# Kernel optimization log

Measured on AMD Instinct MI355X. Metric: run time of the kernel, lower is better.

Reference implementation:

```python
import jax, jax.numpy as jnp
import numpy as np

EPS = 1e-05
N_HEADS = 16
HEAD_DIM = 64

def rms_norm(x, w, eps=EPS):
    # RMSNorm over last dim, computed in float32 then cast back (matches torch source)
    xf = x.astype(jnp.float32)
    out = xf * jax.lax.rsqrt(jnp.mean(xf * xf, axis=-1, keepdims=True) + eps)
    return (out * w).astype(x.dtype)

def split_heads(x, heads):
    # Faithful to reshape_heads: (B,T,C) -> (B,T,C//heads,heads) -> (B,heads,T,C//heads)
    B, T, C = x.shape
    return x.reshape(B, T, C // heads, heads).transpose(0, 3, 1, 2)

def setup_inputs() -> dict:
    key = jax.random.key(0)
    ks = jax.random.split(key, 5)
    B, T, D = 2, 2048, 1024
    s = 0.02
    return {
        "x": jax.random.normal(ks[0], (B, T, D), dtype=jnp.float32),
        "wq": jax.random.normal(ks[1], (D, N_HEADS * HEAD_DIM), dtype=jnp.float32) * s,
        "wk": jax.random.normal(ks[2], (D, N_HEADS * HEAD_DIM), dtype=jnp.float32) * s,
        "wv": jax.random.normal(ks[3], (D, N_HEADS * HEAD_DIM), dtype=jnp.float32) * s,
        "wo": jax.random.normal(ks[4], (N_HEADS * HEAD_DIM, D), dtype=jnp.float32) * s,
        "q_norm_w": jnp.ones((HEAD_DIM,), dtype=jnp.float32),
        "k_norm_w": jnp.ones((HEAD_DIM,), dtype=jnp.float32),
    }

def reference(x, wq, wk, wv, wo, q_norm_w, k_norm_w):
    B, T, D = x.shape
    # QKV projections (no bias)
    q = split_heads(x @ wq, N_HEADS)   # [B,H,T,hd]
    k = split_heads(x @ wk, N_HEADS)
    v = split_heads(x @ wv, N_HEADS)
    # per-head qk RMSNorm
    q = rms_norm(q, q_norm_w)
    k = rms_norm(k, k_norm_w)
    # scaled dot-product attention
    scale = 1.0 / jnp.sqrt(jnp.array(HEAD_DIM, dtype=x.dtype))
    scores = jnp.einsum('bhqd,bhkd->bhqk', q, k) * scale  # [B,H,T,T]
    attn = jax.nn.softmax(scores, axis=-1)
    out = jnp.einsum('bhqk,bhkd->bhqd', attn, v)           # [B,H,T,hd]
    # rearrange 'b h n d -> b n (h d)'
    out = out.transpose(0, 2, 1, 3).reshape(B, T, N_HEADS * HEAD_DIM)
    return out @ wo
```

## Files before the change

### kernel.cpp

```cpp
#include <hip/hip_runtime.h>
#include <hip/hip_fp16.h>

typedef _Float16 f16;
typedef _Float16 f16x8 __attribute__((ext_vector_type(8)));
typedef _Float16 f16x4 __attribute__((ext_vector_type(4)));
typedef float    f32x4 __attribute__((ext_vector_type(4)));

#define DEV __device__ __forceinline__

static constexpr int Tn = 2048;
static constexpr int Dn = 1024;
static constexpr int Hn = 16;
static constexpr int HDn = 64;
static constexpr int Mn = 2 * Tn;
static constexpr int NQKV = 3 * Dn;

DEV void gld16(const void* g, void* l) {
  __builtin_amdgcn_global_load_lds((const __attribute__((address_space(1))) unsigned int*)g,
                                   (__attribute__((address_space(3))) unsigned int*)l, 16, 0, 0);
}

__global__ __launch_bounds__(256) void k_cast_x(const float* __restrict__ x, f16* __restrict__ xb) {
  int i = blockIdx.x * 256 + threadIdx.x;
  float4 v = ((const float4*)x)[i];
  f16x4 o; o.x = (f16)v.x; o.y = (f16)v.y; o.z = (f16)v.z; o.w = (f16)v.w;
  ((f16x4*)xb)[i] = o;
}

__global__ __launch_bounds__(256) void k_wtrans(const float* __restrict__ wq, const float* __restrict__ wk,
                                                const float* __restrict__ wv, const float* __restrict__ wo,
                                                f16* __restrict__ wcat_t, f16* __restrict__ wot) {
  __shared__ float tile[64][65];
  const float* srcs[4] = {wq, wk, wv, wo};
  const float* w = srcs[blockIdx.z];
  f16* dst = (blockIdx.z == 3) ? wot : wcat_t + (size_t)blockIdx.z * Dn * Dn;
  int k0 = blockIdx.x * 64, n0 = blockIdx.y * 64;
#pragma unroll
  for (int p = 0; p < 16; ++p) {
    int flat = threadIdx.x + p * 256;
    int kl = flat >> 6, nl = flat & 63;
    tile[kl][nl] = w[(size_t)(k0 + kl) * Dn + n0 + nl];
  }
  __syncthreads();
#pragma unroll
  for (int p = 0; p < 16; ++p) {
    int flat = threadIdx.x + p * 256;
    int nl = flat >> 6, kl = flat & 63;
    dst[(size_t)(n0 + nl) * Dn + k0 + kl] = (f16)tile[kl][nl];
  }
}

__global__ __launch_bounds__(256) void k_gemm(const f16* __restrict__ A, const f16* __restrict__ Bt,
                                              void* __restrict__ Cout, int N, int K, int out_f16) {
  __shared__ __align__(16) f16 As[128 * 64];
  __shared__ __align__(16) f16 Bs[128 * 64];
  const int lane = threadIdx.x & 63, wid = threadIdx.x >> 6;
  const int m0 = blockIdx.y * 128, n0 = blockIdx.x * 128;
  const int wr = (wid >> 1) * 64, wc = (wid & 1) * 64;
  f32x4 acc[4][4];
#pragma unroll
  for (int i = 0; i < 4; ++i)
#pragma unroll
    for (int j = 0; j < 4; ++j) acc[i][j] = (f32x4){0.f, 0.f, 0.f, 0.f};

  char* AsB = (char*)As; char* BsB = (char*)Bs;
  for (int k0 = 0; k0 < K; k0 += 64) {
    __syncthreads();
#pragma unroll
    for (int it = 0; it < 4; ++it) {
      int flat = ((wid * 4 + it) * 64 + lane) * 16;
      int row = flat >> 7, g = (flat >> 4) & 7;
      int sw = (g ^ (row & 7)) << 4;
      gld16((const char*)A + ((size_t)(m0 + row) * K + k0) * 2 + sw, AsB + (wid * 4 + it) * 1024);
      gld16((const char*)Bt + ((size_t)(n0 + row) * K + k0) * 2 + sw, BsB + (wid * 4 + it) * 1024);
    }
    __syncthreads();
#pragma unroll
    for (int kk = 0; kk < 2; ++kk) {
      f16x8 af[4], bf[4];
#pragma unroll
      for (int ms = 0; ms < 4; ++ms) {
        int r = wr + ms * 16 + (lane & 15);
        af[ms] = *(const f16x8*)(AsB + r * 128 + (((kk * 4 + (lane >> 4)) ^ (r & 7)) << 4));
      }
#pragma unroll
      for (int ns = 0; ns < 4; ++ns) {
        int r = wc + ns * 16 + (lane & 15);
        bf[ns] = *(const f16x8*)(BsB + r * 128 + (((kk * 4 + (lane >> 4)) ^ (r & 7)) << 4));
      }
#pragma unroll
      for (int ms = 0; ms < 4; ++ms)
#pragma unroll
        for (int ns = 0; ns < 4; ++ns)
          acc[ms][ns] = __builtin_amdgcn_mfma_f32_16x16x32_f16(af[ms], bf[ns], acc[ms][ns], 0, 0, 0);
    }
  }
  const int rq = lane >> 4, cq = lane & 15;
  if (out_f16) {
    f16* C = (f16*)Cout;
#pragma unroll
    for (int ms = 0; ms < 4; ++ms)
#pragma unroll
      for (int ns = 0; ns < 4; ++ns)
#pragma unroll
        for (int r = 0; r < 4; ++r)
          C[(size_t)(m0 + wr + ms * 16 + rq * 4 + r) * N + n0 + wc + ns * 16 + cq] = (f16)acc[ms][ns][r];
  } else {
    float* C = (float*)Cout;
#pragma unroll
    for (int ms = 0; ms < 4; ++ms)
#pragma unroll
      for (int ns = 0; ns < 4; ++ns)
#pragma unroll
        for (int r = 0; r < 4; ++r)
          C[(size_t)(m0 + wr + ms * 16 + rq * 4 + r) * N + n0 + wc + ns * 16 + cq] = acc[ms][ns][r];
  }
}

__global__ __launch_bounds__(256) void k_norm(const f16* __restrict__ y, const float* __restrict__ qw,
                                              const float* __restrict__ kw, f16* __restrict__ qatt,
                                              f16* __restrict__ katt, f16* __restrict__ vatt) {
  __shared__ float lq[16][65], lk[16][65], lv[16][65];
  int tg = blockIdx.x;
  int b = tg >> 11, t = tg & 2047;
  const f16* row = y + (size_t)tg * NQKV;
  for (int c = threadIdx.x; c < NQKV; c += 256) {
    float v = (float)row[c];
    int sec = c >> 10, cs = c & 1023;
    float (*dst)[65] = (sec == 0) ? lq : (sec == 1) ? lk : lv;
    dst[cs & 15][cs >> 4] = v;
  }
  __syncthreads();
  int lane = threadIdx.x & 63, wid = threadIdx.x >> 6;
#pragma unroll
  for (int hh = 0; hh < 4; ++hh) {
    int h = wid * 4 + hh;
    float qv = lq[h][lane], kv = lk[h][lane], vv = lv[h][lane];
    float sq = qv * qv, sk = kv * kv;
#pragma unroll
    for (int msk = 1; msk < 64; msk <<= 1) {
      sq += __shfl_xor(sq, msk, 64);
      sk += __shfl_xor(sk, msk, 64);
    }
    float rq = rsqrtf(sq * (1.f / 64) + 1e-5f) * qw[lane] * 0.1803368801111601f;
    float rk = rsqrtf(sk * (1.f / 64) + 1e-5f) * kw[lane];
    size_t obase = (((size_t)(b * 16 + h)) * Tn + t) * 64 + lane;
    qatt[obase] = (f16)(qv * rq);
    katt[obase] = (f16)(kv * rk);
    vatt[obase] = (f16)vv;
  }
}

__global__ __launch_bounds__(256) void k_vtrans(const f16* __restrict__ vatt, f16* __restrict__ vt) {
  __shared__ f16 tile[64][72];
  int t0 = blockIdx.x * 64, bh = blockIdx.y;
  const f16* src = vatt + ((size_t)bh * Tn + t0) * 64;
#pragma unroll
  for (int p = 0; p < 2; ++p) {
    int c = threadIdx.x + p * 256;
    int tl = c >> 3, dc = (c & 7) * 8;
    f16x8 v = *(const f16x8*)(src + (size_t)tl * 64 + dc);
#pragma unroll
    for (int j = 0; j < 8; ++j) tile[dc + j][tl] = v[j];
  }
  __syncthreads();
#pragma unroll
  for (int p = 0; p < 2; ++p) {
    int c = threadIdx.x + p * 256;
    int d = c >> 3, tc = (c & 7) * 8;
    f16x8 o;
#pragma unroll
    for (int j = 0; j < 8; ++j) o[j] = tile[d][tc + j];
    *(f16x8*)(vt + ((size_t)bh * 64 + d) * Tn + t0 + tc) = o;
  }
}

__global__ __launch_bounds__(256) void k_attn(const f16* __restrict__ qatt, const f16* __restrict__ katt,
                                              const f16* __restrict__ vt, f16* __restrict__ attout) {
  __shared__ __align__(16) f16 Ks[2][64 * 64];
  __shared__ __align__(16) f16 Vs[2][64 * 64];
  __shared__ __align__(16) f16 Ps[4][16 * 64];
  const int lane = threadIdx.x & 63, wid = threadIdx.x >> 6;
  const int bh = blockIdx.y, b = bh >> 4, h = bh & 15;
  const int tq0 = blockIdx.x * 64 + wid * 16;

  const f16* qbase = qatt + ((size_t)bh * Tn + tq0) * 64;
  f16x8 qf[2];
#pragma unroll
  for (int kk = 0; kk < 2; ++kk)
    qf[kk] = *(const f16x8*)(qbase + (size_t)(lane & 15) * 64 + kk * 32 + (lane >> 4) * 8);

  f32x4 o[4];
  float psum[4];
#pragma unroll
  for (int i = 0; i < 4; ++i) { o[i] = (f32x4){0.f, 0.f, 0.f, 0.f}; psum[i] = 0.f; }

  const char* kgb = (const char*)(katt + (size_t)bh * Tn * 64);
  const char* vgb = (const char*)(vt + (size_t)bh * 64 * Tn);
  char* KsB = (char*)Ks; char* VsB = (char*)Vs; char* PsB = (char*)Ps[wid];

  auto stage = [&](int buf, int kt) {
    int k0 = kt * 64;
#pragma unroll
    for (int it = 0; it < 2; ++it) {
      int flat = ((wid * 2 + it) * 64 + lane) * 16;
      int row = flat >> 7, g = (flat >> 4) & 7;
      int sw = (g ^ (row & 7)) << 4;
      gld16(kgb + ((size_t)(k0 + row) * 64) * 2 + sw, KsB + buf * 8192 + (wid * 2 + it) * 1024);
      gld16(vgb + ((size_t)row * Tn + k0) * 2 + sw, VsB + buf * 8192 + (wid * 2 + it) * 1024);
    }
  };

  constexpr int NT = Tn / 64;
  stage(0, 0);

  for (int kt = 0; kt < NT; ++kt) {
    const int cur = kt & 1;
    char* Kc = KsB + cur * 8192;
    char* Vc = VsB + cur * 8192;
    if (kt + 1 < NT) {
      stage(cur ^ 1, kt + 1);
      asm volatile("s_waitcnt vmcnt(4)" ::: "memory");
    } else {
      asm volatile("s_waitcnt vmcnt(0)" ::: "memory");
    }
    __builtin_amdgcn_s_barrier();
    __builtin_amdgcn_sched_barrier(0);

    f32x4 s[4];
    __builtin_amdgcn_s_setprio(1);
#pragma unroll
    for (int sub = 0; sub < 4; ++sub) {
      s[sub] = (f32x4){0.f, 0.f, 0.f, 0.f};
#pragma unroll
      for (int kk = 0; kk < 2; ++kk) {
        int kr = sub * 16 + (lane & 15);
        f16x8 kf = *(const f16x8*)(Kc + kr * 128 + (((kk * 4 + (lane >> 4)) ^ (kr & 7)) << 4));
        s[sub] = __builtin_amdgcn_mfma_f32_16x16x32_f16(qf[kk], kf, s[sub], 0, 0, 0);
      }
    }
    __builtin_amdgcn_s_setprio(0);

#pragma unroll
    for (int sub = 0; sub < 4; ++sub)
#pragma unroll
      for (int r = 0; r < 4; ++r) {
        float e = __builtin_amdgcn_exp2f(s[sub][r]);
        psum[r] += e;
        int row = (lane >> 4) * 4 + r;
        int byte = row * 128 + ((((lane & 15) * 2 + sub * 32)) ^ ((row & 7) << 4));
        *(f16*)(PsB + byte) = (f16)e;
      }

    f16x8 pa[2];
#pragma unroll
    for (int kk = 0; kk < 2; ++kk) {
      int row = lane & 15;
      pa[kk] = *(const f16x8*)(PsB + row * 128 + (((kk * 4 + (lane >> 4)) ^ (row & 7)) << 4));
    }
    __builtin_amdgcn_s_setprio(1);
#pragma unroll
    for (int ds = 0; ds < 4; ++ds)
#pragma unroll
      for (int kk = 0; kk < 2; ++kk) {
        int dr = ds * 16 + (lane & 15);
        f16x8 vb = *(const f16x8*)(Vc + dr * 128 + (((kk * 4 + (lane >> 4)) ^ (dr & 7)) << 4));
        o[ds] = __builtin_amdgcn_mfma_f32_16x16x32_f16(pa[kk], vb, o[ds], 0, 0, 0);
      }
    __builtin_amdgcn_s_setprio(0);
    __builtin_amdgcn_s_barrier();
  }

#pragma unroll
  for (int msk = 1; msk < 16; msk <<= 1)
#pragma unroll
    for (int r = 0; r < 4; ++r) psum[r] += __shfl_xor(psum[r], msk, 64);
  float inv[4];
#pragma unroll
  for (int r = 0; r < 4; ++r) inv[r] = 1.f / psum[r];
#pragma unroll
  for (int ds = 0; ds < 4; ++ds)
#pragma unroll
    for (int r = 0; r < 4; ++r) {
      int t = tq0 + (lane >> 4) * 4 + r;
      attout[((size_t)(b * Tn + t)) * Dn + h * 64 + ds * 16 + (lane & 15)] = (f16)(o[ds][r] * inv[r]);
    }
}

extern "C" void kernel_launch(void* const* d_in, const int* in_sizes, int n_in,
                              void* d_out, int out_size, void* d_ws, size_t ws_size,
                              hipStream_t stream) {
  const float* x  = (const float*)d_in[0];
  const float* wq = (const float*)d_in[1];
  const float* wk = (const float*)d_in[2];
  const float* wv = (const float*)d_in[3];
  const float* wo = (const float*)d_in[4];
  const float* qw = (const float*)d_in[5];
  const float* kw = (const float*)d_in[6];

  char* ws = (char*)d_ws;
  const size_t MB = 1 << 20;
  f16* xb     = (f16*)(ws + 0 * MB);
  f16* wcat   = (f16*)(ws + 8 * MB);
  f16* wot    = (f16*)(ws + 14 * MB);
  f16* y      = (f16*)(ws + 16 * MB);
  f16* qatt   = (f16*)(ws + 40 * MB);
  f16* katt   = (f16*)(ws + 48 * MB);
  f16* vatt   = (f16*)(ws + 56 * MB);
  f16* vtb    = (f16*)(ws + 64 * MB);
  f16* attout = (f16*)(ws + 72 * MB);

  k_cast_x<<<dim3(Mn * Dn / 4 / 256), 256, 0, stream>>>(x, xb);
  k_wtrans<<<dim3(16, 16, 4), 256, 0, stream>>>(wq, wk, wv, wo, wcat, wot);
  k_gemm<<<dim3(NQKV / 128, Mn / 128), 256, 0, stream>>>(xb, wcat, (void*)y, NQKV, Dn, 1);
  k_norm<<<dim3(Mn), 256, 0, stream>>>(y, qw, kw, qatt, katt, vatt);
  k_vtrans<<<dim3(Tn / 64, 32), 256, 0, stream>>>(vatt, vtb);
  k_attn<<<dim3(Tn / 64, 32), 256, 0, stream>>>(qatt, katt, vtb, attout);
  k_gemm<<<dim3(Dn / 128, Mn / 128), 256, 0, stream>>>(attout, wot, d_out, Dn, Dn, 0);
}
```

Baseline: 239.1 us.

## Fuse QK RMSNorm into QKV GEMM epilogue, merge prep kernels, retile output GEMM

Merges the x cast and weight transpose into one prep launch. It permutes the QKV weight columns so each GEMM wave owns one head, which lets the RMSNorm and head-split run in the GEMM epilogue and removes the intermediate y buffer and the k_norm kernel. The attention kernel swaps the MFMA operand order so each lane holds one query's row sum, and writes P as packed f16 pairs with the PV loads interleaved. The output GEMM moves to a 64x128 tile to launch more blocks. Risks are epilogue shuffle overhead and uncoalesced scattered f16 stores to the head-major layout.

```diff
diff --git a/kernel.cpp b/kernel.cpp
--- a/kernel.cpp
+++ b/kernel.cpp
@@ -1,5 +1,4 @@
 #include <hip/hip_runtime.h>
-#include <hip/hip_fp16.h>
 
 typedef _Float16 f16;
 typedef _Float16 f16x8 __attribute__((ext_vector_type(8)));
@@ -10,8 +9,6 @@
 
 static constexpr int Tn = 2048;
 static constexpr int Dn = 1024;
-static constexpr int Hn = 16;
-static constexpr int HDn = 64;
 static constexpr int Mn = 2 * Tn;
 static constexpr int NQKV = 3 * Dn;
 
@@ -20,21 +17,31 @@
                                    (__attribute__((address_space(3))) unsigned int*)l, 16, 0, 0);
 }
 
-__global__ __launch_bounds__(256) void k_cast_x(const float* __restrict__ x, f16* __restrict__ xb) {
-  int i = blockIdx.x * 256 + threadIdx.x;
-  float4 v = ((const float4*)x)[i];
-  f16x4 o; o.x = (f16)v.x; o.y = (f16)v.y; o.z = (f16)v.z; o.w = (f16)v.w;
-  ((f16x4*)xb)[i] = o;
-}
-
-__global__ __launch_bounds__(256) void k_wtrans(const float* __restrict__ wq, const float* __restrict__ wk,
-                                                const float* __restrict__ wv, const float* __restrict__ wo,
-                                                f16* __restrict__ wcat_t, f16* __restrict__ wot) {
+DEV void st_pk(void* p, float a, float b) {
+  auto v = __builtin_amdgcn_cvt_pkrtz(a, b);
+  *(unsigned int*)p = __builtin_bit_cast(unsigned int, v);
+}
+
+__global__ __launch_bounds__(256) void k_prep(const float* __restrict__ x, const float* __restrict__ wq,
+                                              const float* __restrict__ wk, const float* __restrict__ wv,
+                                              const float* __restrict__ wo, f16* __restrict__ xb,
+                                              f16* __restrict__ wcat_t, f16* __restrict__ wot) {
+  int bid = blockIdx.x;
+  if (bid < 4096) {
+    int i = bid * 256 + threadIdx.x;
+    float4 v = ((const float4*)x)[i];
+    f16x4 o4; o4.x = (f16)v.x; o4.y = (f16)v.y; o4.z = (f16)v.z; o4.w = (f16)v.w;
+    ((f16x4*)xb)[i] = o4;
+    return;
+  }
   __shared__ float tile[64][65];
+  int wb = bid - 4096;
+  int z = wb >> 8;
+  int rb = wb & 255;
+  int k0 = (rb >> 4) * 64, n0 = (rb & 15) * 64;
   const float* srcs[4] = {wq, wk, wv, wo};
-  const float* w = srcs[blockIdx.z];
-  f16* dst = (blockIdx.z == 3) ? wot : wcat_t + (size_t)blockIdx.z * Dn * Dn;
-  int k0 = blockIdx.x * 64, n0 = blockIdx.y * 64;
+  const float* w = srcs[z];
+  f16* dst = (z == 3) ? wot : wcat_t + (size_t)z * Dn * Dn;
 #pragma unroll
   for (int p = 0; p < 16; ++p) {
     int flat = threadIdx.x + p * 256;
@@ -46,16 +53,22 @@
   for (int p = 0; p < 16; ++p) {
     int flat = threadIdx.x + p * 256;
     int nl = flat >> 6, kl = flat & 63;
-    dst[(size_t)(n0 + nl) * Dn + k0 + kl] = (f16)tile[kl][nl];
-  }
-}
-
-__global__ __launch_bounds__(256) void k_gemm(const f16* __restrict__ A, const f16* __restrict__ Bt,
-                                              void* __restrict__ Cout, int N, int K, int out_f16) {
+    int c = n0 + nl;
+    int cp = (z == 3) ? c : (((c & 15) << 6) | (c >> 4));
+    dst[(size_t)cp * Dn + k0 + kl] = (f16)tile[kl][nl];
+  }
+}
+
+__global__ __launch_bounds__(256) void k_gemm_qkv(const f16* __restrict__ A, const f16* __restrict__ Bt,
+                                                  const float* __restrict__ qw, const float* __restrict__ kw,
+                                                  f16* __restrict__ qatt, f16* __restrict__ katt,
+                                                  f16* __restrict__ vatt) {
+  constexpr int K = 1024;
   __shared__ __align__(16) f16 As[128 * 64];
   __shared__ __align__(16) f16 Bs[128 * 64];
   const int lane = threadIdx.x & 63, wid = threadIdx.x >> 6;
-  const int m0 = blockIdx.y * 128, n0 = blockIdx.x * 128;
+  const int m0 = blockIdx.y * 128;
+  const int n0 = blockIdx.x * 128;
   const int wr = (wid >> 1) * 64, wc = (wid & 1) * 64;
   f32x4 acc[4][4];
 #pragma unroll
@@ -95,59 +108,40 @@
           acc[ms][ns] = __builtin_amdgcn_mfma_f32_16x16x32_f16(af[ms], bf[ns], acc[ms][ns], 0, 0, 0);
     }
   }
+
   const int rq = lane >> 4, cq = lane & 15;
-  if (out_f16) {
-    f16* C = (f16*)Cout;
-#pragma unroll
-    for (int ms = 0; ms < 4; ++ms)
+  const int sec = blockIdx.x >> 3;
+  const int hwave = (((blockIdx.x & 7) * 128) + wc) >> 6;
+  f16* dst = (sec == 0) ? qatt : (sec == 1) ? katt : vatt;
+  float wv[4];
+#pragma unroll
+  for (int ns = 0; ns < 4; ++ns) {
+    if (sec == 0)      wv[ns] = qw[ns * 16 + cq] * 0.18033688011116013f;
+    else if (sec == 1) wv[ns] = kw[ns * 16 + cq];
+    else               wv[ns] = 1.f;
+  }
+#pragma unroll
+  for (int ms = 0; ms < 4; ++ms) {
+#pragma unroll
+    for (int r = 0; r < 4; ++r) {
+      int row = m0 + wr + ms * 16 + rq * 4 + r;
+      float sc = 1.f;
+      if (sec < 2) {
+        float ss = 0.f;
+#pragma unroll
+        for (int ns = 0; ns < 4; ++ns) ss += acc[ms][ns][r] * acc[ms][ns][r];
+        ss += __shfl_xor(ss, 1, 64);
+        ss += __shfl_xor(ss, 2, 64);
+        ss += __shfl_xor(ss, 4, 64);
+        ss += __shfl_xor(ss, 8, 64);
+        sc = rsqrtf(ss * (1.f / 64) + 1e-5f);
+      }
+      int b = row >> 11, t = row & 2047;
+      size_t base = ((size_t)(b * 16 + hwave) * Tn + t) * 64;
 #pragma unroll
       for (int ns = 0; ns < 4; ++ns)
-#pragma unroll
-        for (int r = 0; r < 4; ++r)
-          C[(size_t)(m0 + wr + ms * 16 + rq * 4 + r) * N + n0 + wc + ns * 16 + cq] = (f16)acc[ms][ns][r];
-  } else {
-    float* C = (float*)Cout;
-#pragma unroll
-    for (int ms = 0; ms < 4; ++ms)
-#pragma unroll
-      for (int ns = 0; ns < 4; ++ns)
-#pragma unroll
-        for (int r = 0; r < 4; ++r)
-          C[(size_t)(m0 + wr + ms * 16 + rq * 4 + r) * N + n0 + wc + ns * 16 + cq] = acc[ms][ns][r];
-  }
-}
-
-__global__ __launch_bounds__(256) void k_norm(const f16* __restrict__ y, const float* __restrict__ qw,
-                                              const float* __restrict__ kw, f16* __restrict__ qatt,
-                                              f16* __restrict__ katt, f16* __restrict__ vatt) {
-  __shared__ float lq[16][65], lk[16][65], lv[16][65];
-  int tg = blockIdx.x;
-  int b = tg >> 11, t = tg & 2047;
-  const f16* row = y + (size_t)tg * NQKV;
-  for (int c = threadIdx.x; c < NQKV; c += 256) {
-    float v = (float)row[c];
-    int sec = c >> 10, cs = c & 1023;
-    float (*dst)[65] = (sec == 0) ? lq : (sec == 1) ? lk : lv;
-    dst[cs & 15][cs >> 4] = v;
-  }
-  __syncthreads();
-  int lane = threadIdx.x & 63, wid = threadIdx.x >> 6;
-#pragma unroll
-  for (int hh = 0; hh < 4; ++hh) {
-    int h = wid * 4 + hh;
-    float qv = lq[h][lane], kv = lk[h][lane], vv = lv[h][lane];
-    float sq = qv * qv, sk = kv * kv;
-#pragma unroll
-    for (int msk = 1; msk < 64; msk <<= 1) {
-      sq += __shfl_xor(sq, msk, 64);
-      sk += __shfl_xor(sk, msk, 64);
-    }
-    float rq = rsqrtf(sq * (1.f / 64) + 1e-5f) * qw[lane] * 0.1803368801111601f;
-    float rk = rsqrtf(sk * (1.f / 64) + 1e-5f) * kw[lane];
-    size_t obase = (((size_t)(b * 16 + h)) * Tn + t) * 64 + lane;
-    qatt[obase] = (f16)(qv * rq);
-    katt[obase] = (f16)(kv * rk);
-    vatt[obase] = (f16)vv;
+        dst[base + ns * 16 + cq] = (f16)(acc[ms][ns][r] * sc * wv[ns]);
+    }
   }
 }
 
@@ -179,8 +173,9 @@
                                               const f16* __restrict__ vt, f16* __restrict__ attout) {
   __shared__ __align__(16) f16 Ks[2][64 * 64];
   __shared__ __align__(16) f16 Vs[2][64 * 64];
-  __shared__ __align__(16) f16 Ps[4][16 * 64];
+  __shared__ __align__(16) f16 Ps[4][1024];
   const int lane = threadIdx.x & 63, wid = threadIdx.x >> 6;
+  const int q = lane & 15, g = lane >> 4;
   const int bh = blockIdx.y, b = bh >> 4, h = bh & 15;
   const int tq0 = blockIdx.x * 64 + wid * 16;
 
@@ -188,24 +183,32 @@
   f16x8 qf[2];
 #pragma unroll
   for (int kk = 0; kk < 2; ++kk)
-    qf[kk] = *(const f16x8*)(qbase + (size_t)(lane & 15) * 64 + kk * 32 + (lane >> 4) * 8);
+    qf[kk] = *(const f16x8*)(qbase + (size_t)q * 64 + kk * 32 + g * 8);
 
   f32x4 o[4];
-  float psum[4];
-#pragma unroll
-  for (int i = 0; i < 4; ++i) { o[i] = (f32x4){0.f, 0.f, 0.f, 0.f}; psum[i] = 0.f; }
+#pragma unroll
+  for (int i = 0; i < 4; ++i) o[i] = (f32x4){0.f, 0.f, 0.f, 0.f};
+  float psum = 0.f;
 
   const char* kgb = (const char*)(katt + (size_t)bh * Tn * 64);
   const char* vgb = (const char*)(vt + (size_t)bh * 64 * Tn);
-  char* KsB = (char*)Ks; char* VsB = (char*)Vs; char* PsB = (char*)Ps[wid];
+  char* KsB = (char*)Ks; char* VsB = (char*)Vs;
+  char* PsB = (char*)Ps + wid * 2048;
+  const int xq = (q & 7) << 4;
+  char* pwr[4];
+#pragma unroll
+  for (int sub = 0; sub < 4; ++sub)
+    pwr[sub] = PsB + q * 128 + ((g & 1) * 8) + ((((sub * 2) + (g >> 1)) ^ (q & 7)) << 4);
+  const char* prd0 = PsB + q * 128 + ((g * 16) ^ xq);
+  const char* prd1 = PsB + q * 128 + (((64 + g * 16)) ^ xq);
 
   auto stage = [&](int buf, int kt) {
     int k0 = kt * 64;
 #pragma unroll
     for (int it = 0; it < 2; ++it) {
       int flat = ((wid * 2 + it) * 64 + lane) * 16;
-      int row = flat >> 7, g = (flat >> 4) & 7;
-      int sw = (g ^ (row & 7)) << 4;
+      int row = flat >> 7, gg = (flat >> 4) & 7;
+      int sw = (gg ^ (row & 7)) << 4;
       gld16(kgb + ((size_t)(k0 + row) * 64) * 2 + sw, KsB + buf * 8192 + (wid * 2 + it) * 1024);
       gld16(vgb + ((size_t)row * Tn + k0) * 2 + sw, VsB + buf * 8192 + (wid * 2 + it) * 1024);
     }
@@ -216,8 +219,8 @@
 
   for (int kt = 0; kt < NT; ++kt) {
     const int cur = kt & 1;
-    char* Kc = KsB + cur * 8192;
-    char* Vc = VsB + cur * 8192;
+    const char* Kc = KsB + cur * 8192;
+    const char* Vc = VsB + cur * 8192;
     if (kt + 1 < NT) {
       stage(cur ^ 1, kt + 1);
       asm volatile("s_waitcnt vmcnt(4)" ::: "memory");
@@ -234,57 +237,124 @@
       s[sub] = (f32x4){0.f, 0.f, 0.f, 0.f};
 #pragma unroll
       for (int kk = 0; kk < 2; ++kk) {
-        int kr = sub * 16 + (lane & 15);
-        f16x8 kf = *(const f16x8*)(Kc + kr * 128 + (((kk * 4 + (lane >> 4)) ^ (kr & 7)) << 4));
-        s[sub] = __builtin_amdgcn_mfma_f32_16x16x32_f16(qf[kk], kf, s[sub], 0, 0, 0);
+        int kr = sub * 16 + q;
+        f16x8 kf = *(const f16x8*)(Kc + kr * 128 + (((kk * 4 + g) ^ (kr & 7)) << 4));
+        s[sub] = __builtin_amdgcn_mfma_f32_16x16x32_f16(kf, qf[kk], s[sub], 0, 0, 0);
       }
     }
     __builtin_amdgcn_s_setprio(0);
 
 #pragma unroll
-    for (int sub = 0; sub < 4; ++sub)
-#pragma unroll
-      for (int r = 0; r < 4; ++r) {
-        float e = __builtin_amdgcn_exp2f(s[sub][r]);
-        psum[r] += e;
-        int row = (lane >> 4) * 4 + r;
-        int byte = row * 128 + ((((lane & 15) * 2 + sub * 32)) ^ ((row & 7) << 4));
-        *(f16*)(PsB + byte) = (f16)e;
-      }
-
-    f16x8 pa[2];
-#pragma unroll
-    for (int kk = 0; kk < 2; ++kk) {
-      int row = lane & 15;
-      pa[kk] = *(const f16x8*)(PsB + row * 128 + (((kk * 4 + (lane >> 4)) ^ (row & 7)) << 4));
-    }
+    for (int sub = 0; sub < 2; ++sub) {
+      float e0 = __builtin_amdgcn_exp2f(s[sub][0]);
+      float e1 = __builtin_amdgcn_exp2f(s[sub][1]);
+      float e2 = __builtin_amdgcn_exp2f(s[sub][2]);
+      float e3 = __builtin_amdgcn_exp2f(s[sub][3]);
+      psum += (e0 + e1) + (e2 + e3);
+      st_pk(pwr[sub],     e0, e1);
+      st_pk(pwr[sub] + 4, e2, e3);
+    }
+    f16x8 pa0 = *(const f16x8*)prd0;
+#pragma unroll
+    for (int sub = 2; sub < 4; ++sub) {
+      float e0 = __builtin_amdgcn_exp2f(s[sub][0]);
+      float e1 = __builtin_amdgcn_exp2f(s[sub][1]);
+      float e2 = __builtin_amdgcn_exp2f(s[sub][2]);
+      float e3 = __builtin_amdgcn_exp2f(s[sub][3]);
+      psum += (e0 + e1) + (e2 + e3);
+      st_pk(pwr[sub],     e0, e1);
+      st_pk(pwr[sub] + 4, e2, e3);
+    }
+    f16x8 pa1 = *(const f16x8*)prd1;
+
     __builtin_amdgcn_s_setprio(1);
 #pragma unroll
-    for (int ds = 0; ds < 4; ++ds)
-#pragma unroll
-      for (int kk = 0; kk < 2; ++kk) {
-        int dr = ds * 16 + (lane & 15);
-        f16x8 vb = *(const f16x8*)(Vc + dr * 128 + (((kk * 4 + (lane >> 4)) ^ (dr & 7)) << 4));
-        o[ds] = __builtin_amdgcn_mfma_f32_16x16x32_f16(pa[kk], vb, o[ds], 0, 0, 0);
-      }
+    for (int ds = 0; ds < 4; ++ds) {
+      int dr = ds * 16 + q;
+      f16x8 vb0 = *(const f16x8*)(Vc + dr * 128 + (((0 + g) ^ (dr & 7)) << 4));
+      o[ds] = __builtin_amdgcn_mfma_f32_16x16x32_f16(pa0, vb0, o[ds], 0, 0, 0);
+      f16x8 vb1 = *(const f16x8*)(Vc + dr * 128 + (((4 + g) ^ (dr & 7)) << 4));
+      o[ds] = __builtin_amdgcn_mfma_f32_16x16x32_f16(pa1, vb1, o[ds], 0, 0, 0);
+    }
     __builtin_amdgcn_s_setprio(0);
     __builtin_amdgcn_s_barrier();
   }
 
-#pragma unroll
-  for (int msk = 1; msk < 16; msk <<= 1)
-#pragma unroll
-    for (int r = 0; r < 4; ++r) psum[r] += __shfl_xor(psum[r], msk, 64);
+  psum += __shfl_xor(psum, 16, 64);
+  psum += __shfl_xor(psum, 32, 64);
+  float invq = 1.f / psum;
   float inv[4];
 #pragma unroll
-  for (int r = 0; r < 4; ++r) inv[r] = 1.f / psum[r];
+  for (int r = 0; r < 4; ++r)
+    inv[r] = __int_as_float(__builtin_amdgcn_ds_bpermute(((g * 4 + r)) << 2, __float_as_int(invq)));
 #pragma unroll
   for (int ds = 0; ds < 4; ++ds)
 #pragma unroll
     for (int r = 0; r < 4; ++r) {
-      int t = tq0 + (lane >> 4) * 4 + r;
-      attout[((size_t)(b * Tn + t)) * Dn + h * 64 + ds * 16 + (lane & 15)] = (f16)(o[ds][r] * inv[r]);
-    }
+      int t = tq0 + g * 4 + r;
+      attout[((size_t)(b * Tn + t)) * Dn + h * 64 + ds * 16 + q] = (f16)(o[ds][r] * inv[r]);
+    }
+}
+
+__global__ __launch_bounds__(256) void k_gemm_o(const f16* __restrict__ A, const f16* __restrict__ Bt,
+                                                float* __restrict__ C, int N, int K) {
+  __shared__ __align__(16) f16 As[64 * 64];
+  __shared__ __align__(16) f16 Bs[128 * 64];
+  const int lane = threadIdx.x & 63, wid = threadIdx.x >> 6;
+  const int m0 = blockIdx.y * 64, n0 = blockIdx.x * 128;
+  const int wr = (wid >> 1) * 32, wc = (wid & 1) * 64;
+  f32x4 acc[2][4];
+#pragma unroll
+  for (int i = 0; i < 2; ++i)
+#pragma unroll
+    for (int j = 0; j < 4; ++j) acc[i][j] = (f32x4){0.f, 0.f, 0.f, 0.f};
+
+  char* AsB = (char*)As; char* BsB = (char*)Bs;
+  for (int k0 = 0; k0 < K; k0 += 64) {
+    __syncthreads();
+#pragma unroll
+    for (int it = 0; it < 2; ++it) {
+      int flat = ((wid * 2 + it) * 64 + lane) * 16;
+      int row = flat >> 7, g = (flat >> 4) & 7;
+      int sw = (g ^ (row & 7)) << 4;
+      gld16((const char*)A + ((size_t)(m0 + row) * K + k0) * 2 + sw, AsB + (wid * 2 + it) * 1024);
+    }
+#pragma unroll
+    for (int it = 0; it < 4; ++it) {
+      int flat = ((wid * 4 + it) * 64 + lane) * 16;
+      int row = flat >> 7, g = (flat >> 4) & 7;
+      int sw = (g ^ (row & 7)) << 4;
+      gld16((const char*)Bt + ((size_t)(n0 + row) * K + k0) * 2 + sw, BsB + (wid * 4 + it) * 1024);
+    }
+    __syncthreads();
+#pragma unroll
+    for (int kk = 0; kk < 2; ++kk) {
+      f16x8 af[2], bf[4];
+#pragma unroll
+      for (int ms = 0; ms < 2; ++ms) {
+        int r = wr + ms * 16 + (lane & 15);
+        af[ms] = *(const f16x8*)(AsB + r * 128 + (((kk * 4 + (lane >> 4)) ^ (r & 7)) << 4));
+      }
+#pragma unroll
+      for (int ns = 0; ns < 4; ++ns) {
+        int r = wc + ns * 16 + (lane & 15);
+        bf[ns] = *(const f16x8*)(BsB + r * 128 + (((kk * 4 + (lane >> 4)) ^ (r & 7)) << 4));
+      }
+#pragma unroll
+      for (int ms = 0; ms < 2; ++ms)
+#pragma unroll
+        for (int ns = 0; ns < 4; ++ns)
+          acc[ms][ns] = __builtin_amdgcn_mfma_f32_16x16x32_f16(af[ms], bf[ns], acc[ms][ns], 0, 0, 0);
+    }
+  }
+  const int rq = lane >> 4, cq = lane & 15;
+#pragma unroll
+  for (int ms = 0; ms < 2; ++ms)
+#pragma unroll
+    for (int ns = 0; ns < 4; ++ns)
+#pragma unroll
+      for (int r = 0; r < 4; ++r)
+        C[(size_t)(m0 + wr + ms * 16 + rq * 4 + r) * N + n0 + wc + ns * 16 + cq] = acc[ms][ns][r];
 }
 
 extern "C" void kernel_launch(void* const* d_in, const int* in_sizes, int n_in,
@@ -303,18 +373,15 @@
   f16* xb     = (f16*)(ws + 0 * MB);
   f16* wcat   = (f16*)(ws + 8 * MB);
   f16* wot    = (f16*)(ws + 14 * MB);
-  f16* y      = (f16*)(ws + 16 * MB);
-  f16* qatt   = (f16*)(ws + 40 * MB);
-  f16* katt   = (f16*)(ws + 48 * MB);
-  f16* vatt   = (f16*)(ws + 56 * MB);
-  f16* vtb    = (f16*)(ws + 64 * MB);
-  f16* attout = (f16*)(ws + 72 * MB);
-
-  k_cast_x<<<dim3(Mn * Dn / 4 / 256), 256, 0, stream>>>(x, xb);
-  k_wtrans<<<dim3(16, 16, 4), 256, 0, stream>>>(wq, wk, wv, wo, wcat, wot);
-  k_gemm<<<dim3(NQKV / 128, Mn / 128), 256, 0, stream>>>(xb, wcat, (void*)y, NQKV, Dn, 1);
-  k_norm<<<dim3(Mn), 256, 0, stream>>>(y, qw, kw, qatt, katt, vatt);
+  f16* qatt   = (f16*)(ws + 16 * MB);
+  f16* katt   = (f16*)(ws + 24 * MB);
+  f16* vatt   = (f16*)(ws + 32 * MB);
+  f16* vtb    = (f16*)(ws + 40 * MB);
+  f16* attout = (f16*)(ws + 48 * MB);
+
+  k_prep<<<dim3(5120), 256, 0, stream>>>(x, wq, wk, wv, wo, xb, wcat, wot);
+  k_gemm_qkv<<<dim3(NQKV / 128, Mn / 128), 256, 0, stream>>>(xb, wcat, qw, kw, qatt, katt, vatt);
   k_vtrans<<<dim3(Tn / 64, 32), 256, 0, stream>>>(vatt, vtb);
   k_attn<<<dim3(Tn / 64, 32), 256, 0, stream>>>(qatt, katt, vtb, attout);
-  k_gemm<<<dim3(Dn / 128, Mn / 128), 256, 0, stream>>>(attout, wot, d_out, Dn, Dn, 0);
-}
+  k_gemm_o<<<dim3(Dn / 128, Mn / 64), 256, 0, stream>>>(attout, wot, (float*)d_out, Dn, Dn);
+}
```

Result: faster. 215.1 us (-10.1%).
